# Performance work log

Measured on AMD Instinct MI355X. Metric: run time of the kernel, lower is better.

Reference implementation:

```python
import jax, jax.numpy as jnp
import numpy as np

NUM_HEADS = 4
WINDOW = 3

def setup_inputs() -> dict:
    key = jax.random.key(0)
    ks = jax.random.split(key, 6)
    B, V, C, H, W = 4, 6, 256, 32, 32
    s = 0.02
    return {
        "x": jax.random.normal(ks[0], (B, V, C, H, W), jnp.float32),
        "Wq": jax.random.normal(ks[1], (C, C), jnp.float32) * s,
        "bq": jnp.zeros((C,), jnp.float32),
        "Wk": jax.random.normal(ks[2], (V * C, C), jnp.float32) * s,
        "bk": jnp.zeros((C,), jnp.float32),
        "Wv": jax.random.normal(ks[3], (V * C, C), jnp.float32) * s,
        "bv": jnp.zeros((C,), jnp.float32),
        "Wo": jax.random.normal(ks[4], (C, C), jnp.float32) * s,
        "bo": jnp.zeros((C,), jnp.float32),
    }

def reference(x, Wq, bq, Wk, bk, Wv, bv, Wo, bo):
    B, V, C, H, W = x.shape
    HW = H * W
    S = HW * V  # query sequence length
    nh = NUM_HEADS
    hd = C // nh
    # q: [B, V, H, W, C] -> [B, S, C]
    q_in = jnp.transpose(x, (0, 1, 3, 4, 2)).reshape(B, S, C)
    # k/v input: [B, H, W, V, C] -> [B, HW, V*C]
    kv_in = jnp.transpose(x, (0, 3, 4, 1, 2)).reshape(B, HW, V * C)
    q = q_in @ Wq + bq
    k = kv_in @ Wk + bk
    v = kv_in @ Wv + bv
    q = q.reshape(B, S, nh, hd).transpose(0, 2, 1, 3)    # [B, nh, S, hd]
    k = k.reshape(B, HW, nh, hd).transpose(0, 2, 1, 3)   # [B, nh, HW, hd]
    v = v.reshape(B, HW, nh, hd).transpose(0, 2, 1, 3)   # [B, nh, HW, hd]
    logits = jnp.einsum("bhqd,bhkd->bhqk", q, k) / jnp.sqrt(jnp.float32(hd))
    # Faithful mask: row i has ones in columns [max(0,i-W), i+W] (clipped to HW cols);
    # it is ADDED as mask * -1e9, masking OUT the diagonal window (as in source).
    i = jnp.arange(S)[:, None]
    j = jnp.arange(HW)[None, :]
    mask = ((j >= i - WINDOW) & (j < i + WINDOW + 1)).astype(logits.dtype)
    logits = logits + mask * (-1e9)
    attn = jax.nn.softmax(logits, axis=-1)
    out = jnp.einsum("bhqk,bhkd->bhqd", attn, v)         # [B, nh, S, hd]
    out = out.transpose(0, 2, 1, 3).reshape(B, S, C)
    out = out @ Wo + bo
    return x.reshape(B * V, C, H, W) + out.reshape(B * V, C, H, W)
```

## Files before the change

### kernel.cpp

```cpp
#include <hip/hip_runtime.h>
#include <cstddef>

namespace {

constexpr int B=4, V=6, C=256, HWS=1024, S=6144, NH=4, HD=64, VC=1536;

typedef short short8  __attribute__((ext_vector_type(8)));
typedef short short4v __attribute__((ext_vector_type(4)));
typedef float f32x4   __attribute__((ext_vector_type(4)));

__device__ inline short f2bf(float f){
  union{float f; unsigned u;} v; v.f=f;
  unsigned r = v.u + 0x7fffu + ((v.u>>16)&1u);
  return (short)(r>>16);
}
__device__ inline unsigned fbits(float f){
  union{float f; unsigned u;} v; v.f=f; return v.u;
}

__device__ inline void tr_tile(const float* in, int inRow, short* out, int outRow,
                               int r0, int c0, short* T , int t){
  {
    const int rr=t>>2, cc=(t&3)*16;
    const float* p = in + (size_t)(r0+rr)*inRow + c0 + cc;
    short tmp[16];
    #pragma unroll
    for(int j=0;j<4;j++){
      const float4 f=*(const float4*)(p+j*4);
      tmp[j*4+0]=f2bf(f.x); tmp[j*4+1]=f2bf(f.y);
      tmp[j*4+2]=f2bf(f.z); tmp[j*4+3]=f2bf(f.w);
    }
    *(short8*)&T[rr*72+cc]   = *(short8*)&tmp[0];
    *(short8*)&T[rr*72+cc+8] = *(short8*)&tmp[8];
  }
  __syncthreads();
  {
    const int cc=t>>2, rr0=(t&3)*16;
    short tmp[16];
    #pragma unroll
    for(int j=0;j<16;j++) tmp[j]=T[(rr0+j)*72+cc];
    short* o = out + (size_t)(c0+cc)*outRow + r0 + rr0;
    *(short8*)o     = *(short8*)&tmp[0];
    *(short8*)(o+8) = *(short8*)&tmp[8];
  }
}

__global__ __launch_bounds__(256) void prep(const float* __restrict__ x,
                                            const float* __restrict__ Wq, const float* __restrict__ Wk,
                                            const float* __restrict__ Wv, const float* __restrict__ Wo,
                                            short* __restrict__ xb, short* __restrict__ WqT,
                                            short* __restrict__ WkT, short* __restrict__ WvT,
                                            short* __restrict__ WoT){
  __shared__ short T[64*72];
  const int blk=blockIdx.x;
  if(blk<1536){
    const int bx=blk&15, by=(blk>>4)&3, bv=blk>>6;
    tr_tile(x + (size_t)bv*C*HWS, HWS, xb + (size_t)bv*HWS*C, C, by*64, bx*64, T, threadIdx.x);
  } else {
    const int idx=blk-1536;
    const int tile=idx%96, z=idx/96;
    const float* in; short* out; int R;
    if(z==0){in=Wq; out=WqT; R=C;}
    else if(z==1){in=Wo; out=WoT; R=C;}
    else if(z==2){in=Wk; out=WkT; R=VC;}
    else         {in=Wv; out=WvT; R=VC;}
    const int tilesC=C/64, ntiles=(R/64)*tilesC;
    if(tile>=ntiles) return;
    tr_tile(in, C, out, R, (tile/tilesC)*64, (tile%tilesC)*64, T, threadIdx.x);
  }
}

template<int MODE>
__device__ inline void qo_body(const short* __restrict__ A, const short* __restrict__ BT,
                               const float* __restrict__ bias, const float* __restrict__ xres,
                               void* __restrict__ outv, short* As, short* Bs, int n0, int r0){
  const int t=threadIdx.x, lane=t&63, w=t>>6, quad=lane>>4, ln=lane&15;
  f32x4 acc[2][4];
  #pragma unroll
  for(int rt=0;rt<2;rt++)
    #pragma unroll
    for(int nt=0;nt<4;nt++) acc[rt][nt]=(f32x4)0.f;

  for(int k0=0;k0<C;k0+=64){
    if(k0) __syncthreads();
    { const int r=t>>1, c=(t&1)*32;
      const short* p = A + (size_t)(r0+r)*C + k0 + c;
      #pragma unroll
      for(int j=0;j<4;j++) *(short8*)&As[r*72+c+j*8] = *(const short8*)(p+j*8);
    }
    { const int n=t>>2, c=(t&3)*16;
      const short* p = BT + (size_t)(n0+n)*C + k0 + c;
      *(short8*)&Bs[n*72+c]   = *(const short8*)p;
      *(short8*)&Bs[n*72+c+8] = *(const short8*)(p+8);
    }
    __syncthreads();
    #pragma unroll
    for(int s=0;s<2;s++){
      short8 af0=*(short8*)&As[(w*32+ln)*72    + s*32+quad*8];
      short8 af1=*(short8*)&As[(w*32+16+ln)*72 + s*32+quad*8];
      #pragma unroll
      for(int nt=0;nt<4;nt++){
        const short8 bf=*(short8*)&Bs[(nt*16+ln)*72 + s*32+quad*8];
        acc[0][nt]=__builtin_amdgcn_mfma_f32_16x16x32_bf16(af0,bf,acc[0][nt],0,0,0);
        acc[1][nt]=__builtin_amdgcn_mfma_f32_16x16x32_bf16(af1,bf,acc[1][nt],0,0,0);
      }
    }
  }

  constexpr float QSCALE = 0.18033688011112042f;
  float bcol[4];
  #pragma unroll
  for(int nt=0;nt<4;nt++) bcol[nt]=bias[n0+nt*16+ln];
  #pragma unroll
  for(int rt=0;rt<2;rt++)
    #pragma unroll
    for(int nt=0;nt<4;nt++)
      #pragma unroll
      for(int i=0;i<4;i++){
        const int row=r0+w*32+rt*16+quad*4+i, col=n0+nt*16+ln;
        const float vv=acc[rt][nt][i]+bcol[nt];
        if constexpr(MODE==0) ((short*)outv)[(size_t)row*C+col]=f2bf(vv*QSCALE);
        else ((float*)outv)[(size_t)row*C+col]=vv + xres[(size_t)row*C+col];
      }
}

__global__ __launch_bounds__(256) void proj(const short* __restrict__ xb,
                                            const short* __restrict__ WqT, const short* __restrict__ WkT,
                                            const short* __restrict__ WvT,
                                            const float* __restrict__ bq, const float* __restrict__ bk,
                                            const float* __restrict__ bv,
                                            short* __restrict__ qb, short* __restrict__ Kpack,
                                            short* __restrict__ Vpack){
  __shared__ __align__(16) short sh[13824];
  const int blk=blockIdx.x;
  const int t=threadIdx.x, lane=t&63, w=t>>6, quad=lane>>4, ln=lane&15;

  if(blk>=256){
    const int qblk=blk-256;
    qo_body<0>(xb, WqT, bq, nullptr, qb, sh, sh+9216, (qblk&3)*64, (qblk>>2)*128);
    return;
  }

  short* As=sh; short* Bk=sh+4608; short* Bv=sh+9216;
  const int n0=(blk&3)*64, r0=(blk>>2)*64;
  const int b=r0>>10, hw0=r0&1023;
  const int h=n0>>6, bh=b*NH+h;

  f32x4 ak[4], av[4];
  #pragma unroll
  for(int nt=0;nt<4;nt++){ ak[nt]=(f32x4)0.f; av[nt]=(f32x4)0.f; }

  const int sr=t>>2, sc=(t&3)*16;
  for(int k0=0;k0<VC;k0+=64){
    if(k0) __syncthreads();
    const int v=k0>>8, c0=k0&255;
    { const short* p = xb + (size_t)((b*V+v)*HWS + hw0+sr)*C + c0 + sc;
      *(short8*)&As[sr*72+sc]   = *(const short8*)p;
      *(short8*)&As[sr*72+sc+8] = *(const short8*)(p+8); }
    { const short* p = WkT + (size_t)(n0+sr)*VC + k0 + sc;
      *(short8*)&Bk[sr*72+sc]   = *(const short8*)p;
      *(short8*)&Bk[sr*72+sc+8] = *(const short8*)(p+8); }
    { const short* p = WvT + (size_t)(n0+sr)*VC + k0 + sc;
      *(short8*)&Bv[sr*72+sc]   = *(const short8*)p;
      *(short8*)&Bv[sr*72+sc+8] = *(const short8*)(p+8); }
    __syncthreads();
    #pragma unroll
    for(int s=0;s<2;s++){
      const short8 af=*(short8*)&As[(w*16+ln)*72 + s*32+quad*8];
      #pragma unroll
      for(int nt=0;nt<4;nt++){
        const short8 kf=*(short8*)&Bk[(nt*16+ln)*72 + s*32+quad*8];
        const short8 vf=*(short8*)&Bv[(nt*16+ln)*72 + s*32+quad*8];
        ak[nt]=__builtin_amdgcn_mfma_f32_16x16x32_bf16(af,kf,ak[nt],0,0,0);
        av[nt]=__builtin_amdgcn_mfma_f32_16x16x32_bf16(af,vf,av[nt],0,0,0);
      }
    }
  }

  float bkc[4], bvc[4];
  #pragma unroll
  for(int nt=0;nt<4;nt++){ bkc[nt]=bk[n0+nt*16+ln]; bvc[nt]=bv[n0+nt*16+ln]; }

  {
    short* vq = Vpack + ((size_t)(bh*64 + (hw0>>4) + w))*1024;
    #pragma unroll
    for(int nt=0;nt<4;nt++){
      short4v vp;
      #pragma unroll
      for(int i=0;i<4;i++) vp[i]=f2bf(av[nt][i]+bvc[nt]);
      *(short4v*)(vq + nt*256 + lane*4) = vp;
    }
  }

  __syncthreads();
  #pragma unroll
  for(int nt=0;nt<4;nt++)
    #pragma unroll
    for(int i=0;i<4;i++)
      As[(w*16+quad*4+i)*72 + nt*16+ln] = f2bf(ak[nt][i]+bkc[nt]);
  __syncthreads();
  {
    short* kp = Kpack + ((size_t)(bh*64 + (hw0>>4) + w))*1024;
    #pragma unroll
    for(int half=0; half<2; half++){
      const short8 f = *(short8*)&As[(w*16+ln)*72 + half*32 + quad*8];
      *(short8*)(kp + half*512 + lane*8) = f;
    }
  }
}

__global__ __launch_bounds__(256) void attn_k(const short* __restrict__ q, const short* __restrict__ Kpack,
                                              const short* __restrict__ Vpack, short* __restrict__ ao){
  __shared__ float obuf[64*68];
  __shared__ float lbuf[4][64];
  const int blk=blockIdx.x;
  const int bh=(blk&7)*2 + ((blk>>3)&1);
  const int qt=blk>>4;
  const int b=bh>>2, h=bh&3;
  const int s0=qt*64;
  const int t=threadIdx.x, lane=t&63, w=t>>6, quad=lane>>4, ln=lane&15;

  short8 qf[4][2];
  #pragma unroll
  for(int nt=0;nt<4;nt++)
    #pragma unroll
    for(int s=0;s<2;s++)
      qf[nt][s]=*(const short8*)&q[(size_t)(b*S+s0+nt*16+ln)*C + h*HD + s*32+quad*8];

  f32x4 o[4][4];
  #pragma unroll
  for(int dt=0;dt<4;dt++)
    #pragma unroll
    for(int nt=0;nt<4;nt++) o[dt][nt]=(f32x4)0.f;
  f32x4 l4[4];
  #pragma unroll
  for(int nt=0;nt<4;nt++) l4[nt]=(f32x4)0.f;

  const short* kbase = Kpack + ((size_t)(bh*64+w))*1024;
  const short* vbase = Vpack + ((size_t)(bh*64+w))*1024;
  const f32x4 z4=(f32x4)0.f;

  short8 kfa0=*(const short8*)(kbase + lane*8);
  short8 kfa1=*(const short8*)(kbase + 512 + lane*8);
  short8 kfb0=*(const short8*)(kbase + 4096 + lane*8);
  short8 kfb1=*(const short8*)(kbase + 4096 + 512 + lane*8);

#define ATTN_TILE(KF0,KF1,TI,PI)                                              \
  {                                                                           \
    const short* vp = vbase + (size_t)(TI)*4096;                              \
    short4v vf[4];                                                            \
    _Pragma("unroll")                                                         \
    for(int dt=0;dt<4;dt++) vf[dt]=*(const short4v*)(vp + dt*256 + lane*4);   \
    f32x4 sa[4];                                                              \
    _Pragma("unroll")                                                         \
    for(int nt=0;nt<4;nt++){                                                  \
      sa[nt]=__builtin_amdgcn_mfma_f32_16x16x32_bf16(KF0,qf[nt][0],z4,0,0,0); \
      sa[nt]=__builtin_amdgcn_mfma_f32_16x16x32_bf16(KF1,qf[nt][1],sa[nt],0,0,0); \
    }                                                                         \
    const size_t poff=(size_t)(PI)*4096;                                      \
    KF0=*(const short8*)(kbase + poff + lane*8);                              \
    KF1=*(const short8*)(kbase + poff + 512 + lane*8);                        \
    const int kmin=(TI)*64 + w*16;                                            \
    if(kmin+15 >= s0-3 && kmin <= s0+66){                                     \
      _Pragma("unroll")                                                       \
      for(int nt=0;nt<4;nt++){                                                \
        const int ig=s0+nt*16+ln;                                             \
        _Pragma("unroll")                                                     \
        for(int i=0;i<4;i++){                                                 \
          const int jg=kmin+quad*4+i;                                         \
          if((unsigned)(jg-ig+3)<=6u) sa[nt][i]=-100.f;                       \
        }                                                                     \
      }                                                                       \
    }                                                                         \
    short4v pt[4];                                                            \
    _Pragma("unroll")                                                         \
    for(int nt=0;nt<4;nt++){                                                  \
      f32x4 pv;                                                               \
      _Pragma("unroll")                                                       \
      for(int i=0;i<4;i++) pv[i]=__builtin_amdgcn_exp2f(sa[nt][i]);           \
      l4[nt]+=pv;                                                             \
      union{ short4v s; unsigned u[2]; } P;                                   \
      P.u[0]=__builtin_amdgcn_perm(fbits(pv[1]), fbits(pv[0]), 0x07060302u);  \
      P.u[1]=__builtin_amdgcn_perm(fbits(pv[3]), fbits(pv[2]), 0x07060302u);  \
      pt[nt]=P.s;                                                             \
    }                                                                         \
    _Pragma("unroll")                                                         \
    for(int dt=0;dt<4;dt++)                                                   \
      _Pragma("unroll")                                                       \
      for(int nt=0;nt<4;nt++)                                                 \
        o[dt][nt]=__builtin_amdgcn_mfma_f32_16x16x16bf16_1k(vf[dt],pt[nt],o[dt][nt],0,0,0); \
  }

  #pragma unroll 1
  for(int i=0;i<16;i+=2){
    const int ipa = (i+2<16)? i+2 : i;
    const int ipb = (i+3<16)? i+3 : i+1;
    ATTN_TILE(kfa0,kfa1,i,ipa)
    ATTN_TILE(kfb0,kfb1,i+1,ipb)
  }
#undef ATTN_TILE

  float l[4];
  #pragma unroll
  for(int nt=0;nt<4;nt++){
    l[nt]=l4[nt][0]+l4[nt][1]+l4[nt][2]+l4[nt][3];
    l[nt]+=__shfl_xor(l[nt],16);
    l[nt]+=__shfl_xor(l[nt],32);
  }
  if(quad==0){
    #pragma unroll
    for(int nt=0;nt<4;nt++) lbuf[w][nt*16+ln]=l[nt];
  }
  for(int r=0;r<4;r++){
    if(w==r){
      #pragma unroll
      for(int dt=0;dt<4;dt++)
        #pragma unroll
        for(int nt=0;nt<4;nt++)
          #pragma unroll
          for(int i=0;i<4;i++){
            const int idx=(dt*16+quad*4+i)*68 + nt*16+ln;
            if(r==0) obuf[idx]=o[dt][nt][i]; else obuf[idx]+=o[dt][nt][i];
          }
    }
    __syncthreads();
  }

  {
    const int row=t>>2, dg=t&3;
    const float linv=1.0f/(lbuf[0][row]+lbuf[1][row]+lbuf[2][row]+lbuf[3][row]);
    short tmp[16];
    #pragma unroll
    for(int j=0;j<16;j++) tmp[j]=f2bf(obuf[(dg*16+j)*68+row]*linv);
    short* op = ao + (size_t)(b*S+s0+row)*C + h*HD + dg*16;
    *(short8*)op     = *(short8*)&tmp[0];
    *(short8*)(op+8) = *(short8*)&tmp[8];
  }
}

__global__ __launch_bounds__(256) void o_gemm(const short* __restrict__ A, const short* __restrict__ BT,
                                              const float* __restrict__ bias, const float* __restrict__ xres,
                                              float* __restrict__ out){
  __shared__ __align__(16) short sh[13824];
  qo_body<1>(A, BT, bias, xres, out, sh, sh+9216, (int)(blockIdx.x&3)*64, (int)(blockIdx.x>>2)*128);
}

}

extern "C" void kernel_launch(void* const* d_in, const int* in_sizes, int n_in,
                              void* d_out, int out_size, void* d_ws, size_t ws_size,
                              hipStream_t stream) {
  const float* x  = (const float*)d_in[0];
  const float* Wq = (const float*)d_in[1];
  const float* bq = (const float*)d_in[2];
  const float* Wk = (const float*)d_in[3];
  const float* bk = (const float*)d_in[4];
  const float* Wv = (const float*)d_in[5];
  const float* bv = (const float*)d_in[6];
  const float* Wo = (const float*)d_in[7];
  const float* bo = (const float*)d_in[8];
  float* out = (float*)d_out;

  char* p = (char*)d_ws;
  const size_t szBS=(size_t)B*S*C*2, szK=(size_t)B*HWS*C*2;
  short* xb   =(short*)p; p+=szBS;
  short* qb   =(short*)p; p+=szBS;
  short* aob  =(short*)p; p+=szBS;
  short* Kpack=(short*)p; p+=szK;
  short* Vpack=(short*)p; p+=szK;
  short* WqT=(short*)p; p+=(size_t)C*C*2;
  short* WoT=(short*)p; p+=(size_t)C*C*2;
  short* WkT=(short*)p; p+=(size_t)C*VC*2;
  short* WvT=(short*)p; p+=(size_t)C*VC*2;

  prep<<<dim3(1920), 256, 0, stream>>>(x, Wq,Wk,Wv,Wo, xb, WqT,WkT,WvT,WoT);
  proj<<<dim3(1024), 256, 0, stream>>>(xb, WqT,WkT,WvT, bq,bk,bv, qb, Kpack, Vpack);
  attn_k<<<dim3(B*NH*(S/64)), 256, 0, stream>>>(qb, Kpack, Vpack, aob);
  o_gemm<<<dim3(4*((B*S)/128)), 256, 0, stream>>>(aob, WoT, bo, x, out);
}
```

Before: 196.3 us.

## Split attention waves 2x2 over query and key halves, cut reduction syncs

Reassigns the four waves in the attention block from splitting only over keys (each wave covering all 64 queries) to a 2x2 split over query halves and key halves. Each wave now holds half the Q fragments and output accumulators, which lowers register pressure, and the launch bounds ask for four blocks per CU. The cross-wave output reduction shrinks from four serialized sync rounds to two. In exchange the explicit K-fragment double-buffer prefetch is dropped and each wave reads 32 keys per tile instead of 16, so per-wave load latency may be less hidden.

```diff
diff --git a/kernel.cpp b/kernel.cpp
--- a/kernel.cpp
+++ b/kernel.cpp
@@ -209,126 +209,138 @@
   }
 }
 
-__global__ __launch_bounds__(256) void attn_k(const short* __restrict__ q, const short* __restrict__ Kpack,
-                                              const short* __restrict__ Vpack, short* __restrict__ ao){
+__global__ __launch_bounds__(256,4) void attn_k(const short* __restrict__ q, const short* __restrict__ Kpack,
+                                                const short* __restrict__ Vpack, short* __restrict__ ao){
   __shared__ float obuf[64*68];
-  __shared__ float lbuf[4][64];
+  __shared__ float lbuf[4][32];
   const int blk=blockIdx.x;
   const int bh=(blk&7)*2 + ((blk>>3)&1);
   const int qt=blk>>4;
   const int b=bh>>2, h=bh&3;
   const int s0=qt*64;
   const int t=threadIdx.x, lane=t&63, w=t>>6, quad=lane>>4, ln=lane&15;
-
-  short8 qf[4][2];
-  #pragma unroll
-  for(int nt=0;nt<4;nt++)
+  const int wq=w&1, wk=w>>1;
+
+  short8 qf[2][2];
+  #pragma unroll
+  for(int ntl=0;ntl<2;ntl++)
     #pragma unroll
     for(int s=0;s<2;s++)
-      qf[nt][s]=*(const short8*)&q[(size_t)(b*S+s0+nt*16+ln)*C + h*HD + s*32+quad*8];
-
-  f32x4 o[4][4];
+      qf[ntl][s]=*(const short8*)&q[(size_t)(b*S+s0+(wq*2+ntl)*16+ln)*C + h*HD + s*32+quad*8];
+
+  f32x4 o[4][2];
   #pragma unroll
   for(int dt=0;dt<4;dt++)
     #pragma unroll
-    for(int nt=0;nt<4;nt++) o[dt][nt]=(f32x4)0.f;
-  f32x4 l4[4];
-  #pragma unroll
-  for(int nt=0;nt<4;nt++) l4[nt]=(f32x4)0.f;
-
-  const short* kbase = Kpack + ((size_t)(bh*64+w))*1024;
-  const short* vbase = Vpack + ((size_t)(bh*64+w))*1024;
+    for(int ntl=0;ntl<2;ntl++) o[dt][ntl]=(f32x4)0.f;
+  f32x4 l4[2];
+  l4[0]=(f32x4)0.f; l4[1]=(f32x4)0.f;
+
+  const short* kbase = Kpack + ((size_t)bh*64 + wk*2)*1024;
+  const short* vbase = Vpack + ((size_t)bh*64 + wk*2)*1024;
   const f32x4 z4=(f32x4)0.f;
-
-  short8 kfa0=*(const short8*)(kbase + lane*8);
-  short8 kfa1=*(const short8*)(kbase + 512 + lane*8);
-  short8 kfb0=*(const short8*)(kbase + 4096 + lane*8);
-  short8 kfb1=*(const short8*)(kbase + 4096 + 512 + lane*8);
-
-#define ATTN_TILE(KF0,KF1,TI,PI)                                              \
-  {                                                                           \
-    const short* vp = vbase + (size_t)(TI)*4096;                              \
-    short4v vf[4];                                                            \
-    _Pragma("unroll")                                                         \
-    for(int dt=0;dt<4;dt++) vf[dt]=*(const short4v*)(vp + dt*256 + lane*4);   \
-    f32x4 sa[4];                                                              \
-    _Pragma("unroll")                                                         \
-    for(int nt=0;nt<4;nt++){                                                  \
-      sa[nt]=__builtin_amdgcn_mfma_f32_16x16x32_bf16(KF0,qf[nt][0],z4,0,0,0); \
-      sa[nt]=__builtin_amdgcn_mfma_f32_16x16x32_bf16(KF1,qf[nt][1],sa[nt],0,0,0); \
-    }                                                                         \
-    const size_t poff=(size_t)(PI)*4096;                                      \
-    KF0=*(const short8*)(kbase + poff + lane*8);                              \
-    KF1=*(const short8*)(kbase + poff + 512 + lane*8);                        \
-    const int kmin=(TI)*64 + w*16;                                            \
-    if(kmin+15 >= s0-3 && kmin <= s0+66){                                     \
-      _Pragma("unroll")                                                       \
-      for(int nt=0;nt<4;nt++){                                                \
-        const int ig=s0+nt*16+ln;                                             \
-        _Pragma("unroll")                                                     \
-        for(int i=0;i<4;i++){                                                 \
-          const int jg=kmin+quad*4+i;                                         \
-          if((unsigned)(jg-ig+3)<=6u) sa[nt][i]=-100.f;                       \
-        }                                                                     \
-      }                                                                       \
-    }                                                                         \
-    short4v pt[4];                                                            \
-    _Pragma("unroll")                                                         \
-    for(int nt=0;nt<4;nt++){                                                  \
-      f32x4 pv;                                                               \
-      _Pragma("unroll")                                                       \
-      for(int i=0;i<4;i++) pv[i]=__builtin_amdgcn_exp2f(sa[nt][i]);           \
-      l4[nt]+=pv;                                                             \
-      union{ short4v s; unsigned u[2]; } P;                                   \
-      P.u[0]=__builtin_amdgcn_perm(fbits(pv[1]), fbits(pv[0]), 0x07060302u);  \
-      P.u[1]=__builtin_amdgcn_perm(fbits(pv[3]), fbits(pv[2]), 0x07060302u);  \
-      pt[nt]=P.s;                                                             \
-    }                                                                         \
-    _Pragma("unroll")                                                         \
-    for(int dt=0;dt<4;dt++)                                                   \
-      _Pragma("unroll")                                                       \
-      for(int nt=0;nt<4;nt++)                                                 \
-        o[dt][nt]=__builtin_amdgcn_mfma_f32_16x16x16bf16_1k(vf[dt],pt[nt],o[dt][nt],0,0,0); \
-  }
+  const int rb = s0 + wq*32;
 
   #pragma unroll 1
-  for(int i=0;i<16;i+=2){
-    const int ipa = (i+2<16)? i+2 : i;
-    const int ipb = (i+3<16)? i+3 : i+1;
-    ATTN_TILE(kfa0,kfa1,i,ipa)
-    ATTN_TILE(kfb0,kfb1,i+1,ipb)
-  }
-#undef ATTN_TILE
-
-  float l[4];
-  #pragma unroll
-  for(int nt=0;nt<4;nt++){
-    l[nt]=l4[nt][0]+l4[nt][1]+l4[nt][2]+l4[nt][3];
-    l[nt]+=__shfl_xor(l[nt],16);
-    l[nt]+=__shfl_xor(l[nt],32);
-  }
-  if(quad==0){
-    #pragma unroll
-    for(int nt=0;nt<4;nt++) lbuf[w][nt*16+ln]=l[nt];
-  }
-  for(int r=0;r<4;r++){
-    if(w==r){
+  for(int TI=0; TI<16; TI++){
+    const short* kp = kbase + (size_t)TI*4096;
+    const short* vp = vbase + (size_t)TI*4096;
+    const short8 kf00=*(const short8*)(kp + lane*8);
+    const short8 kf01=*(const short8*)(kp + 512 + lane*8);
+    const short8 kf10=*(const short8*)(kp + 1024 + lane*8);
+    const short8 kf11=*(const short8*)(kp + 1536 + lane*8);
+
+    f32x4 sa[2][2];
+    #pragma unroll
+    for(int ntl=0;ntl<2;ntl++){
+      sa[0][ntl]=__builtin_amdgcn_mfma_f32_16x16x32_bf16(kf00,qf[ntl][0],z4,0,0,0);
+      sa[0][ntl]=__builtin_amdgcn_mfma_f32_16x16x32_bf16(kf01,qf[ntl][1],sa[0][ntl],0,0,0);
+      sa[1][ntl]=__builtin_amdgcn_mfma_f32_16x16x32_bf16(kf10,qf[ntl][0],z4,0,0,0);
+      sa[1][ntl]=__builtin_amdgcn_mfma_f32_16x16x32_bf16(kf11,qf[ntl][1],sa[1][ntl],0,0,0);
+    }
+
+    short4v vf[2][4];
+    #pragma unroll
+    for(int kt=0;kt<2;kt++)
       #pragma unroll
       for(int dt=0;dt<4;dt++)
-        #pragma unroll
-        for(int nt=0;nt<4;nt++)
+        vf[kt][dt]=*(const short4v*)(vp + kt*1024 + dt*256 + lane*4);
+
+    const int kmin=TI*64 + wk*32;
+    if(kmin+31 >= rb-3 && kmin <= rb+34){
+      #pragma unroll
+      for(int kt=0;kt<2;kt++)
+        #pragma unroll
+        for(int ntl=0;ntl<2;ntl++){
+          const int ig=rb+ntl*16+ln;
           #pragma unroll
           for(int i=0;i<4;i++){
-            const int idx=(dt*16+quad*4+i)*68 + nt*16+ln;
-            if(r==0) obuf[idx]=o[dt][nt][i]; else obuf[idx]+=o[dt][nt][i];
+            const int jg=kmin+kt*16+quad*4+i;
+            if((unsigned)(jg-ig+3)<=6u) sa[kt][ntl][i]=-100.f;
           }
-    }
-    __syncthreads();
-  }
+        }
+    }
+
+    short4v pt[2][2];
+    #pragma unroll
+    for(int kt=0;kt<2;kt++)
+      #pragma unroll
+      for(int ntl=0;ntl<2;ntl++){
+        f32x4 pv;
+        #pragma unroll
+        for(int i=0;i<4;i++) pv[i]=__builtin_amdgcn_exp2f(sa[kt][ntl][i]);
+        l4[ntl]+=pv;
+        union{ short4v s; unsigned u[2]; } P;
+        P.u[0]=__builtin_amdgcn_perm(fbits(pv[1]), fbits(pv[0]), 0x07060302u);
+        P.u[1]=__builtin_amdgcn_perm(fbits(pv[3]), fbits(pv[2]), 0x07060302u);
+        pt[kt][ntl]=P.s;
+      }
+
+    #pragma unroll
+    for(int kt=0;kt<2;kt++)
+      #pragma unroll
+      for(int dt=0;dt<4;dt++)
+        #pragma unroll
+        for(int ntl=0;ntl<2;ntl++)
+          o[dt][ntl]=__builtin_amdgcn_mfma_f32_16x16x16bf16_1k(vf[kt][dt],pt[kt][ntl],o[dt][ntl],0,0,0);
+  }
+
+  float l[2];
+  #pragma unroll
+  for(int ntl=0;ntl<2;ntl++){
+    l[ntl]=l4[ntl][0]+l4[ntl][1]+l4[ntl][2]+l4[ntl][3];
+    l[ntl]+=__shfl_xor(l[ntl],16);
+    l[ntl]+=__shfl_xor(l[ntl],32);
+  }
+  if(quad==0){
+    lbuf[w][ln]    = l[0];
+    lbuf[w][16+ln] = l[1];
+  }
+  if(wk==0){
+    #pragma unroll
+    for(int dt=0;dt<4;dt++)
+      #pragma unroll
+      for(int ntl=0;ntl<2;ntl++)
+        #pragma unroll
+        for(int i=0;i<4;i++)
+          obuf[(dt*16+quad*4+i)*68 + wq*32+ntl*16+ln] = o[dt][ntl][i];
+  }
+  __syncthreads();
+  if(wk==1){
+    #pragma unroll
+    for(int dt=0;dt<4;dt++)
+      #pragma unroll
+      for(int ntl=0;ntl<2;ntl++)
+        #pragma unroll
+        for(int i=0;i<4;i++)
+          obuf[(dt*16+quad*4+i)*68 + wq*32+ntl*16+ln] += o[dt][ntl][i];
+  }
+  __syncthreads();
 
   {
     const int row=t>>2, dg=t&3;
-    const float linv=1.0f/(lbuf[0][row]+lbuf[1][row]+lbuf[2][row]+lbuf[3][row]);
+    const int wqr=row>>5, idx=row&31;
+    const float linv=1.0f/(lbuf[wqr][idx]+lbuf[wqr+2][idx]);
     short tmp[16];
     #pragma unroll
     for(int j=0;j<16;j++) tmp[j]=f2bf(obuf[(dg*16+j)*68+row]*linv);
```

After: 190.2 us. -3.1%, faster.
